# Performance work log

Measured on AMD Instinct MI355X. Metric: run time of the kernel, lower is better.

## Reference

```python
import jax, jax.numpy as jnp
import numpy as np

K_IN = 9      # input_patch_size
K_OUT = 3     # output_patch_size
C_IN = 4      # nb_of_input_features
C_OUT = 2     # nb_of_output_features
HID = 50      # int_layer_width
B, H, W = 16, 128, 128
CUT = K_IN // 2 - K_OUT // 2  # border pixels cut from output (3)


def _unfold(x, k):
    # x: [B, C, H, W] -> [B, C*k*k, L] with torch unfold ordering (c, ki, kj)
    b, c, h, w = x.shape
    ho, wo = h - k + 1, w - k + 1
    cols = jnp.stack([x[:, :, i:i + ho, j:j + wo]
                      for i in range(k) for j in range(k)], axis=2)  # [B,C,k*k,ho,wo]
    return cols.reshape(b, c * k * k, ho * wo)


def _fold_add(patches, oh, ow):
    # patches: [B, C, k, k, ho, wo] -> overlap-add into [B, C, oh, ow]
    b, c, k, _, ho, wo = patches.shape
    out = jnp.zeros((b, c, oh, ow), dtype=patches.dtype)
    for i in range(k):
        for j in range(k):
            out = out.at[:, :, i:i + ho, j:j + wo].add(patches[:, :, i, j])
    return out


def setup_inputs() -> dict:
    key = jax.random.key(0)
    ks = jax.random.split(key, 7)
    f_in = C_IN * K_IN * K_IN      # 324
    f_out = C_OUT * K_OUT * K_OUT  # 18
    s1 = 1.0 / np.sqrt(f_in)
    s2 = 1.0 / np.sqrt(HID)
    return {
        "x": jax.random.normal(ks[0], (B, C_IN, H, W), dtype=jnp.float32),
        "W1": jax.random.uniform(ks[1], (f_in, HID), jnp.float32, -s1, s1),
        "b1": jax.random.uniform(ks[2], (HID,), jnp.float32, -s1, s1),
        "W2": jax.random.uniform(ks[3], (HID, HID), jnp.float32, -s2, s2),
        "b2": jax.random.uniform(ks[4], (HID,), jnp.float32, -s2, s2),
        "W3": jax.random.uniform(ks[5], (HID, f_out), jnp.float32, -s2, s2),
        "b3": jax.random.uniform(ks[6], (f_out,), jnp.float32, -s2, s2),
    }


def reference(x, W1, b1, W2, b2, W3, b3):
    b, c, h, w = x.shape
    oh, ow = h - 2 * CUT, w - 2 * CUT          # 122, 122
    ho, wo = h - K_IN + 1, w - K_IN + 1        # 120, 120 (= oh-K_OUT+1)
    # unfold -> [B, L, C_in*K_in^2] -> flatten rows
    cols = _unfold(x, K_IN)                    # [B, 324, L]
    feats = cols.transpose(0, 2, 1).reshape(b * ho * wo, -1)
    # 3-layer MLP
    hmid = jax.nn.relu(feats @ W1 + b1)
    hmid = jax.nn.relu(hmid @ W2 + b2)
    out = hmid @ W3 + b3                       # [B*L, C_out*K_out^2]
    # fold (overlap-add), torch feature ordering (c, ki, kj)
    patches = out.reshape(b, ho, wo, C_OUT, K_OUT, K_OUT)
    patches = patches.transpose(0, 3, 4, 5, 1, 2)  # [B, C_out, k, k, ho, wo]
    res = _fold_add(patches, oh, ow)
    # divisor = fold(unfold(ones)) -> per-pixel overlap count
    ones_patches = jnp.ones((1, 1, K_OUT, K_OUT, ho, wo), dtype=x.dtype)
    divisor = _fold_add(ones_patches, oh, ow)  # [1,1,oh,ow]
    return res / divisor
```

## Files before the change

kernel.cpp:

```cpp
#include <hip/hip_runtime.h>
#include <hip/hip_bf16.h>

#define BATCH   16
#define C_INF   4
#define H_IN    128
#define W_IN    128
#define HID     50
#define F_OUT   18
#define HO      120
#define WO      120
#define OH      122
#define OW      122
#define NPOS    (BATCH * HO * WO)
#define MBLK    128
#define NBLKS   (NPOS / MBLK)
#define NXCD    8

#define NB1     (11*4*64*8)
#define NB2     (2*4*64*8)
#define NB3     (2*2*64*8)
#define NWF     (NB1 + NB2 + NB3)
#define WOFF    (NPOS * F_OUT)
#define NXC     (BATCH * C_INF * H_IN * W_IN)
#define PREP_BLOCKS  ((NWF + 255) / 256)
#define XCONV_BLOCKS (NXC / (256 * 8))
#define CW      16
#define NSTG    (36*512)

typedef float    v4f     __attribute__((ext_vector_type(4)));
typedef short    short4v __attribute__((ext_vector_type(4)));
typedef short    short8  __attribute__((ext_vector_type(8)));
typedef _Float16 v8hf    __attribute__((ext_vector_type(8)));
typedef int      v4i     __attribute__((ext_vector_type(4)));
typedef short8 short8_a4 __attribute__((aligned(4)));

__device__ inline short f2h(float x) {
    _Float16 h = (_Float16)x;
    return __builtin_bit_cast(short, h);
}
__device__ inline float h2f(short s) {
    return (float)__builtin_bit_cast(_Float16, s);
}

__device__ inline int hswz(int m, int j) {
    return (m * 64 + j) ^ ((m & 7) << 3);
}

__device__ inline int slot_to_k1(int s, int qb, int e) {
    if (s < 9) {
        int pair = s*4 + qb;
        int c = pair/9, ki = pair - c*9;
        return c*81 + ki*9 + e;
    }
    int r = (s-9)*32 + qb*8 + e;
    if (r >= 36) return -1;
    int c = r/9, ki = r - c*9;
    return c*81 + ki*9 + 8;
}

__global__ __launch_bounds__(256)
void prep_kernel(const float* __restrict__ x,
                 const float* __restrict__ W1, const float* __restrict__ W2,
                 const float* __restrict__ W3, short* __restrict__ wf,
                 short* __restrict__ xe, short* __restrict__ xo)
{
    const int blk = blockIdx.x;
    if (blk >= PREP_BLOCKS) {
        const int j = ((blk - PREP_BLOCKS)*256 + (int)threadIdx.x) * 8;
        v4f a = *(const v4f*)&x[j];
        v4f b = *(const v4f*)&x[j + 4];
        float c9 = (j + 8 < NXC) ? x[j + 8] : 0.f;
        short s[9];
        #pragma unroll
        for (int e = 0; e < 4; ++e) { s[e] = f2h(a[e]); s[e+4] = f2h(b[e]); }
        s[8] = f2h(c9);
        short8 ve, vo;
        #pragma unroll
        for (int e = 0; e < 8; ++e) { ve[e] = s[e]; vo[e] = s[e+1]; }
        *(short8*)&xe[j] = ve;
        *(short8*)&xo[j] = vo;
        return;
    }
    int i = blk * 256 + threadIdx.x;
    if (i >= NWF) return;
    float val;
    if (i < NB1) {
        int t = i;
        int e = t & 7, lane = (t >> 3) & 63;
        int rest = t >> 9;
        int u = rest & 3, s = rest >> 2;
        int k = slot_to_k1(s, lane >> 4, e);
        int n = u*16 + (lane & 15);
        val = (k >= 0 && n < HID) ? W1[k*HID + n] : 0.f;
    } else if (i < NB1 + NB2) {
        int t = i - NB1;
        int e = t & 7, lane = (t >> 3) & 63;
        int rest = t >> 9;
        int u = rest & 3, s = rest >> 2;
        int k = s*32 + ((lane >> 4) << 3) + e;
        int n = u*16 + (lane & 15);
        val = (k < HID && n < HID) ? W2[k*HID + n] : 0.f;
    } else {
        int t = i - NB1 - NB2;
        int e = t & 7, lane = (t >> 3) & 63;
        int rest = t >> 9;
        int u = rest & 1, s = rest >> 1;
        int k = s*32 + ((lane >> 4) << 3) + e;
        int n = u*16 + (lane & 15);
        val = (k < HID && n < F_OUT) ? W3[k*F_OUT + n] : 0.f;
    }
    wf[i] = f2h(val);
}

__global__ __launch_bounds__(256, 3)
void mfma_mlp(const short* __restrict__ xe, const short* __restrict__ xo,
              const float* __restrict__ b1, const float* __restrict__ b2,
              const float* __restrict__ b3,
              const short* __restrict__ wf, short* __restrict__ out3)
{
    __shared__ short wlds[NSTG];
    __shared__ short h_lds[128 * 64];

    const int tid  = threadIdx.x;
    const int lane = tid & 63;
    const int w    = tid >> 6;
    const int q    = lane >> 4, col = lane & 15;
    const int swz   = (blockIdx.x & 7) * (NBLKS / NXCD) + (blockIdx.x >> 3);
    const int mbase = swz * MBLK;
    const int mw    = w * 32;

    #pragma unroll
    for (int it = 0; it < 9; ++it) {
        const int cbase = it*256 + w*64;
        const short* g  = wf + (cbase + lane)*8;
        __builtin_amdgcn_global_load_lds(
            (const __attribute__((address_space(1))) void*)g,
            (__attribute__((address_space(3))) void*)&wlds[cbase*8],
            16, 0, 0);
    }

    float bias1[4], bias2[4], bias3[2];
    #pragma unroll
    for (int u = 0; u < 4; ++u) {
        int j = u*16 + col;
        bias1[u] = (j < HID) ? b1[j] : 0.f;
        bias2[u] = (j < HID) ? b2[j] : 0.f;
    }
    #pragma unroll
    for (int u = 0; u < 2; ++u) {
        int j = u*16 + col;
        bias3[u] = (j < F_OUT) ? b3[j] : 0.f;
    }

    const short* xp[2];
    #pragma unroll
    for (int t = 0; t < 2; ++t) {
        int pos = mbase + mw + t*16 + col;
        int b   = pos / (HO*WO); int rem = pos - b*(HO*WO);
        int y   = rem / WO;      int xc  = rem - y*WO;
        int bi  = b*(C_INF*H_IN*W_IN) + y*W_IN + xc;
        xp[t] = (bi & 1) ? (xo + (bi - 1)) : (xe + bi);
    }

    const v4i* B1L = (const v4i*)wf + lane;
    const v4i* B2L = (const v4i*)(wf + NB1) + lane;
    const v4i* B3L = (const v4i*)(wf + NB1 + NB2) + lane;

    __syncthreads();

    v4f acc[2][4];
    #pragma unroll
    for (int t = 0; t < 2; ++t)
        #pragma unroll
        for (int u = 0; u < 4; ++u)
            acc[t][u] = (v4f){0.f, 0.f, 0.f, 0.f};

    #pragma unroll
    for (int s = 0; s < 9; ++s) {
        const int pair = s*4 + q;
        const int c = pair/9, ki = pair - c*9;
        const int off = c*(H_IN*W_IN) + ki*W_IN;

        short8 ah[2];
        #pragma unroll
        for (int t = 0; t < 2; ++t)
            ah[t] = *(const short8_a4*)(xp[t] + off);

        #pragma unroll
        for (int u = 0; u < 4; ++u) {
            v4i bv = *(const v4i*)&wlds[((s*4 + u)*64 + lane)*8];
            v8hf bh = __builtin_bit_cast(v8hf, bv);
            #pragma unroll
            for (int t = 0; t < 2; ++t) {
                v8hf a_h = __builtin_bit_cast(v8hf, ah[t]);
                acc[t][u] = __builtin_amdgcn_mfma_f32_16x16x32_f16(a_h, bh, acc[t][u], 0, 0, 0);
            }
        }
    }
    #pragma unroll
    for (int sr = 0; sr < 2; ++sr) {
        const int s = 9 + sr;
        short8 ah[2];
        #pragma unroll
        for (int e = 0; e < 8; ++e) {
            int r = sr*32 + q*8 + e;
            bool valid = (r < 36);
            int c = valid ? r/9 : 0;
            int ki = r - c*9;
            int off = c*(H_IN*W_IN) + ki*W_IN + 8;
            #pragma unroll
            for (int t = 0; t < 2; ++t)
                ah[t][e] = valid ? xp[t][off] : (short)0;
        }
        #pragma unroll
        for (int u = 0; u < 4; ++u) {
            v8hf bh = __builtin_bit_cast(v8hf, B1L[(s*4 + u)*64]);
            #pragma unroll
            for (int t = 0; t < 2; ++t) {
                v8hf a_h = __builtin_bit_cast(v8hf, ah[t]);
                acc[t][u] = __builtin_amdgcn_mfma_f32_16x16x32_f16(a_h, bh, acc[t][u], 0, 0, 0);
            }
        }
    }

    #pragma unroll
    for (int u = 0; u < 4; ++u) {
        #pragma unroll
        for (int t = 0; t < 2; ++t) {
            #pragma unroll
            for (int r = 0; r < 4; ++r) {
                float v = fmaxf(acc[t][u][r] + bias1[u], 0.f);
                int m = mw + t*16 + q*4 + r;
                h_lds[hswz(m, u*16 + col)] = f2h(v);
            }
        }
    }

    v4f acc2[2][4];
    #pragma unroll
    for (int t = 0; t < 2; ++t)
        #pragma unroll
        for (int u = 0; u < 4; ++u)
            acc2[t][u] = (v4f){0.f, 0.f, 0.f, 0.f};

    #pragma unroll
    for (int s = 0; s < 2; ++s) {
        short8 ah2[2];
        #pragma unroll
        for (int t = 0; t < 2; ++t) {
            int m = mw + t*16 + col;
            ah2[t] = *(const short8*)&h_lds[hswz(m, s*32 + q*8)];
        }
        #pragma unroll
        for (int u = 0; u < 4; ++u) {
            v8hf bh = __builtin_bit_cast(v8hf, B2L[(s*4 + u)*64]);
            #pragma unroll
            for (int t = 0; t < 2; ++t) {
                v8hf a_h = __builtin_bit_cast(v8hf, ah2[t]);
                acc2[t][u] = __builtin_amdgcn_mfma_f32_16x16x32_f16(a_h, bh, acc2[t][u], 0, 0, 0);
            }
        }
    }

    #pragma unroll
    for (int u = 0; u < 4; ++u) {
        #pragma unroll
        for (int t = 0; t < 2; ++t) {
            #pragma unroll
            for (int r = 0; r < 4; ++r) {
                float v = fmaxf(acc2[t][u][r] + bias2[u], 0.f);
                int m = mw + t*16 + q*4 + r;
                h_lds[hswz(m, u*16 + col)] = f2h(v);
            }
        }
    }

    v4f acc3[2][2];
    #pragma unroll
    for (int t = 0; t < 2; ++t)
        #pragma unroll
        for (int u = 0; u < 2; ++u)
            acc3[t][u] = (v4f){0.f, 0.f, 0.f, 0.f};

    #pragma unroll
    for (int s = 0; s < 2; ++s) {
        short8 ah3[2];
        #pragma unroll
        for (int t = 0; t < 2; ++t) {
            int m = mw + t*16 + col;
            ah3[t] = *(const short8*)&h_lds[hswz(m, s*32 + q*8)];
        }
        #pragma unroll
        for (int u = 0; u < 2; ++u) {
            v8hf bh = __builtin_bit_cast(v8hf, B3L[(s*2 + u)*64]);
            #pragma unroll
            for (int t = 0; t < 2; ++t) {
                v8hf a_h = __builtin_bit_cast(v8hf, ah3[t]);
                acc3[t][u] = __builtin_amdgcn_mfma_f32_16x16x32_f16(a_h, bh, acc3[t][u], 0, 0, 0);
            }
        }
    }

    #pragma unroll
    for (int u = 0; u < 2; ++u) {
        int j = u*16 + col;
        if (j < F_OUT) {
            #pragma unroll
            for (int t = 0; t < 2; ++t) {
                short4v vs;
                #pragma unroll
                for (int r = 0; r < 4; ++r) vs[r] = f2h(acc3[t][u][r] + bias3[u]);
                __builtin_nontemporal_store(vs,
                    (short4v*)&out3[j*NPOS + mbase + mw + t*16 + q*4]);
            }
        }
    }
}

__global__ __launch_bounds__(256)
void fold_kernel(const short* __restrict__ out3, float* __restrict__ out)
{
    const int idx = blockIdx.x * 256 + threadIdx.x;
    const int total = BATCH * 2 * OH * CW;
    if (idx >= total) return;

    int t = idx;
    const int cx = t % CW; t /= CW;
    const int oy = t % OH; t /= OH;
    const int c  = t & 1;  t >>= 1;
    const int b  = t;
    const int ox0 = cx * 8;

    if (oy >= 2 && oy < HO && cx >= 1 && cx <= 14) {
        float accv[8];
        #pragma unroll
        for (int e = 0; e < 8; ++e) accv[e] = 0.f;
        #pragma unroll
        for (int ki = 0; ki < 3; ++ki) {
            const int y    = oy - ki;
            const int rowb = (b*HO + y)*WO;
            const int ob   = (c*3 + ki)*3;
            short8 v0 = *(const short8_a4*)&out3[(ob + 0)*NPOS + rowb + ox0];
            short8 v1 = *(const short8_a4*)&out3[(ob + 1)*NPOS + rowb + ox0 - 2];
            int   v1b = *(const int*)      &out3[(ob + 1)*NPOS + rowb + ox0 + 6];
            short8 v2 = *(const short8_a4*)&out3[(ob + 2)*NPOS + rowb + ox0 - 2];
            #pragma unroll
            for (int e = 0; e < 8; ++e) {
                accv[e] += h2f(v0[e]);
                accv[e] += (e < 7) ? h2f(v1[e + 1]) : h2f((short)(v1b & 0xffff));
                accv[e] += h2f(v2[e]);
            }
        }
        float* op = &out[((b*2 + c)*OH + oy)*OW + ox0];
        #pragma unroll
        for (int e = 0; e < 8; ++e) op[e] = accv[e] / 9.f;
        return;
    }

    #pragma unroll
    for (int e = 0; e < 8; ++e) {
        const int ox = ox0 + e;
        if (ox < OW) {
            const int ylo = max(0, oy - 2), yhi = min(HO - 1, oy);
            const int xlo = max(0, ox - 2), xhi = min(WO - 1, ox);
            float s = 0.f;
            for (int y = ylo; y <= yhi; ++y) {
                const int ki = oy - y;
                for (int xx = xlo; xx <= xhi; ++xx) {
                    const int kj = ox - xx;
                    const int o  = (c*3 + ki)*3 + kj;
                    s += h2f(out3[o*NPOS + (b*HO + y)*WO + xx]);
                }
            }
            const float div = (float)((yhi - ylo + 1) * (xhi - xlo + 1));
            out[((b*2 + c)*OH + oy)*OW + ox] = s / div;
        }
    }
}

extern "C" void kernel_launch(void* const* d_in, const int* in_sizes, int n_in,
                              void* d_out, int out_size, void* d_ws, size_t ws_size,
                              hipStream_t stream)
{
    const float* x  = (const float*)d_in[0];
    const float* W1 = (const float*)d_in[1];
    const float* b1 = (const float*)d_in[2];
    const float* W2 = (const float*)d_in[3];
    const float* b2 = (const float*)d_in[4];
    const float* W3 = (const float*)d_in[5];
    const float* b3 = (const float*)d_in[6];

    short* out3 = (short*)d_ws;
    short* wf   = out3 + WOFF;
    short* xe   = wf + NWF;
    short* xo   = xe + NXC;

    prep_kernel<<<PREP_BLOCKS + XCONV_BLOCKS, 256, 0, stream>>>(x, W1, W2, W3, wf, xe, xo);

    mfma_mlp<<<NBLKS, 256, 0, stream>>>(xe, xo, b1, b2, b3, wf, out3);

    const int total = BATCH * 2 * OH * CW;
    fold_kernel<<<(total + 255) / 256, 256, 0, stream>>>(out3, (float*)d_out);
}
```

Before: 114.0 us.

## Prefetch all layer-1 activations and layer-2/3 weights into registers upfront

Hoists all layer-1 A-operand global loads before the weight staging and barrier, so they are issued together and their latency overlaps the LDS weight copy. The full layer-1 weight block (all 11 slots) is now staged into LDS, and layer-2/3 weights are preloaded into registers before the layer-1 epilogue. Empty asm statements pin the loaded values so the compiler keeps the loads early. In exchange, register and LDS use grow a lot, so launch bounds drop from 3 to 2 waves per SIMD, lowering occupancy.

New measurement: 116.6 us. 1.02x slower.

```diff
diff --git a/kernel.cpp b/kernel.cpp
--- a/kernel.cpp
+++ b/kernel.cpp
@@ -25,7 +25,6 @@
 #define PREP_BLOCKS  ((NWF + 255) / 256)
 #define XCONV_BLOCKS (NXC / (256 * 8))
 #define CW      16
-#define NSTG    (36*512)
 
 typedef float    v4f     __attribute__((ext_vector_type(4)));
 typedef short    short4v __attribute__((ext_vector_type(4)));
@@ -40,6 +39,12 @@
 }
 __device__ inline float h2f(short s) {
     return (float)__builtin_bit_cast(_Float16, s);
+}
+__device__ inline void keepv(short8 x) {
+    asm volatile("" :: "v"(__builtin_bit_cast(v4i, x)));
+}
+__device__ inline void keepi(v4i x) {
+    asm volatile("" :: "v"(x));
 }
 
 __device__ inline int hswz(int m, int j) {
@@ -112,13 +117,13 @@
     wf[i] = f2h(val);
 }
 
-__global__ __launch_bounds__(256, 3)
+__global__ __launch_bounds__(256, 2)
 void mfma_mlp(const short* __restrict__ xe, const short* __restrict__ xo,
               const float* __restrict__ b1, const float* __restrict__ b2,
               const float* __restrict__ b3,
               const short* __restrict__ wf, short* __restrict__ out3)
 {
-    __shared__ short wlds[NSTG];
+    __shared__ short wlds[NB1];
     __shared__ short h_lds[128 * 64];
 
     const int tid  = threadIdx.x;
@@ -129,8 +134,44 @@
     const int mbase = swz * MBLK;
     const int mw    = w * 32;
 
-    #pragma unroll
-    for (int it = 0; it < 9; ++it) {
+    const short* xp[2];
+    #pragma unroll
+    for (int t = 0; t < 2; ++t) {
+        int pos = mbase + mw + t*16 + col;
+        int b   = pos / (HO*WO); int rem = pos - b*(HO*WO);
+        int y   = rem / WO;      int xc  = rem - y*WO;
+        int bi  = b*(C_INF*H_IN*W_IN) + y*W_IN + xc;
+        xp[t] = (bi & 1) ? (xo + (bi - 1)) : (xe + bi);
+    }
+
+    short8 ah[9][2];
+    #pragma unroll
+    for (int s = 0; s < 9; ++s) {
+        const int pair = s*4 + q;
+        const int c = pair/9, ki = pair - c*9;
+        const int off = c*(H_IN*W_IN) + ki*W_IN;
+        #pragma unroll
+        for (int t = 0; t < 2; ++t)
+            ah[s][t] = *(const short8_a4*)(xp[t] + off);
+    }
+    short8 ahr[2][2];
+    #pragma unroll
+    for (int sr = 0; sr < 2; ++sr) {
+        #pragma unroll
+        for (int e = 0; e < 8; ++e) {
+            int r = sr*32 + q*8 + e;
+            bool valid = (r < 36);
+            int c = valid ? r/9 : 0;
+            int ki = r - c*9;
+            int off = c*(H_IN*W_IN) + ki*W_IN + 8;
+            #pragma unroll
+            for (int t = 0; t < 2; ++t)
+                ahr[sr][t][e] = valid ? xp[t][off] : (short)0;
+        }
+    }
+
+    #pragma unroll
+    for (int it = 0; it < 11; ++it) {
         const int cbase = it*256 + w*64;
         const short* g  = wf + (cbase + lane)*8;
         __builtin_amdgcn_global_load_lds(
@@ -152,20 +193,14 @@
         bias3[u] = (j < F_OUT) ? b3[j] : 0.f;
     }
 
-    const short* xp[2];
-    #pragma unroll
-    for (int t = 0; t < 2; ++t) {
-        int pos = mbase + mw + t*16 + col;
-        int b   = pos / (HO*WO); int rem = pos - b*(HO*WO);
-        int y   = rem / WO;      int xc  = rem - y*WO;
-        int bi  = b*(C_INF*H_IN*W_IN) + y*W_IN + xc;
-        xp[t] = (bi & 1) ? (xo + (bi - 1)) : (xe + bi);
-    }
-
-    const v4i* B1L = (const v4i*)wf + lane;
     const v4i* B2L = (const v4i*)(wf + NB1) + lane;
     const v4i* B3L = (const v4i*)(wf + NB1 + NB2) + lane;
 
+    #pragma unroll
+    for (int s = 0; s < 9; ++s) { keepv(ah[s][0]); keepv(ah[s][1]); }
+    #pragma unroll
+    for (int sr = 0; sr < 2; ++sr) { keepv(ahr[sr][0]); keepv(ahr[sr][1]); }
+
     __syncthreads();
 
     v4f acc[2][4];
@@ -177,22 +212,13 @@
 
     #pragma unroll
     for (int s = 0; s < 9; ++s) {
-        const int pair = s*4 + q;
-        const int c = pair/9, ki = pair - c*9;
-        const int off = c*(H_IN*W_IN) + ki*W_IN;
-
-        short8 ah[2];
-        #pragma unroll
-        for (int t = 0; t < 2; ++t)
-            ah[t] = *(const short8_a4*)(xp[t] + off);
-
         #pragma unroll
         for (int u = 0; u < 4; ++u) {
             v4i bv = *(const v4i*)&wlds[((s*4 + u)*64 + lane)*8];
             v8hf bh = __builtin_bit_cast(v8hf, bv);
             #pragma unroll
             for (int t = 0; t < 2; ++t) {
-                v8hf a_h = __builtin_bit_cast(v8hf, ah[t]);
+                v8hf a_h = __builtin_bit_cast(v8hf, ah[s][t]);
                 acc[t][u] = __builtin_amdgcn_mfma_f32_16x16x32_f16(a_h, bh, acc[t][u], 0, 0, 0);
             }
         }
@@ -200,28 +226,27 @@
     #pragma unroll
     for (int sr = 0; sr < 2; ++sr) {
         const int s = 9 + sr;
-        short8 ah[2];
-        #pragma unroll
-        for (int e = 0; e < 8; ++e) {
-            int r = sr*32 + q*8 + e;
-            bool valid = (r < 36);
-            int c = valid ? r/9 : 0;
-            int ki = r - c*9;
-            int off = c*(H_IN*W_IN) + ki*W_IN + 8;
-            #pragma unroll
-            for (int t = 0; t < 2; ++t)
-                ah[t][e] = valid ? xp[t][off] : (short)0;
-        }
         #pragma unroll
         for (int u = 0; u < 4; ++u) {
-            v8hf bh = __builtin_bit_cast(v8hf, B1L[(s*4 + u)*64]);
+            v4i bv = *(const v4i*)&wlds[((s*4 + u)*64 + lane)*8];
+            v8hf bh = __builtin_bit_cast(v8hf, bv);
             #pragma unroll
             for (int t = 0; t < 2; ++t) {
-                v8hf a_h = __builtin_bit_cast(v8hf, ah[t]);
+                v8hf a_h = __builtin_bit_cast(v8hf, ahr[sr][t]);
                 acc[t][u] = __builtin_amdgcn_mfma_f32_16x16x32_f16(a_h, bh, acc[t][u], 0, 0, 0);
             }
         }
     }
+
+    v4i b2r[8], b3r[4];
+    #pragma unroll
+    for (int i = 0; i < 8; ++i) b2r[i] = B2L[i*64];
+    #pragma unroll
+    for (int i = 0; i < 4; ++i) b3r[i] = B3L[i*64];
+    #pragma unroll
+    for (int i = 0; i < 8; ++i) keepi(b2r[i]);
+    #pragma unroll
+    for (int i = 0; i < 4; ++i) keepi(b3r[i]);
 
     #pragma unroll
     for (int u = 0; u < 4; ++u) {
@@ -253,7 +278,7 @@
         }
         #pragma unroll
         for (int u = 0; u < 4; ++u) {
-            v8hf bh = __builtin_bit_cast(v8hf, B2L[(s*4 + u)*64]);
+            v8hf bh = __builtin_bit_cast(v8hf, b2r[s*4 + u]);
             #pragma unroll
             for (int t = 0; t < 2; ++t) {
                 v8hf a_h = __builtin_bit_cast(v8hf, ah2[t]);
@@ -292,7 +317,7 @@
         }
         #pragma unroll
         for (int u = 0; u < 2; ++u) {
-            v8hf bh = __builtin_bit_cast(v8hf, B3L[(s*2 + u)*64]);
+            v8hf bh = __builtin_bit_cast(v8hf, b3r[s*2 + u]);
             #pragma unroll
             for (int t = 0; t < 2; ++t) {
                 v8hf a_h = __builtin_bit_cast(v8hf, ah3[t]);
```
